# Optimization experiments

Hardware: AMD Instinct MI355X
Metric: run time of the kernel (lower is better)

The kernel has to match this reference:

```python
import jax, jax.numpy as jnp
import numpy as np

S, T, N, D, H, DT = 4, 4, 65536, 128, 128, 128


def setup_inputs() -> dict:
    key = jax.random.key(0)
    ks = jax.random.split(key, 9)
    inv_d = 1.0 / np.sqrt(D)
    inv_h = 1.0 / np.sqrt(H)
    return {
        "states": jax.random.normal(ks[0], (N, D), dtype=jnp.float32),
        "scores": jax.random.uniform(ks[1], (N, 1), dtype=jnp.float32),
        "type_ids": jax.random.randint(ks[2], (N,), 0, S, dtype=jnp.int32),
        "type_matching": jax.random.normal(ks[3], (S, T), dtype=jnp.float32),
        "W1": jax.random.normal(ks[4], (S, T, D, H), dtype=jnp.float32) * inv_d,
        "b1": jnp.zeros((S, T, H), dtype=jnp.float32),
        "W2": jax.random.normal(ks[5], (S, T, H, DT), dtype=jnp.float32) * inv_h,
        "b2": jnp.zeros((S, T, DT), dtype=jnp.float32),
        "C1": jax.random.normal(ks[6], (S, T, D, H), dtype=jnp.float32) * inv_d,
        "c1": jnp.zeros((S, T, H), dtype=jnp.float32),
        "C2": jax.random.normal(ks[7], (S, T, H, 1), dtype=jnp.float32) * inv_h,
        "c2": jnp.zeros((S, T, 1), dtype=jnp.float32),
    }


def reference(states, scores, type_ids, type_matching, W1, b1, W2, b2, C1, c1, C2, c2):
    """Batched MetaphorMorphism.forward with best_match_only=True.

    For each item with source type s: route to t* = argmax sigmoid(type_matching[s]),
    apply mapper MLP (D->H->DT, ReLU), classifier MLP (D->H->1, ReLU, sigmoid),
    new_score = min(score, classifier_out), item_prob = sigmoid(type_matching)[s, t*].
    """
    match_sig = jax.nn.sigmoid(type_matching)          # [S, T]
    best_t = jnp.argmax(type_matching, axis=1)         # [S] (argmax of sigmoid == argmax of logits)
    best_prob = match_sig[jnp.arange(S), best_t]       # [S]

    out_state = jnp.zeros((states.shape[0], W2.shape[-1]), dtype=states.dtype)
    out_score = jnp.zeros_like(scores)
    # loop over the small, fixed set of source types (structurally distinct experts)
    for s in range(S):
        t = best_t[s]
        h = jax.nn.relu(states @ W1[s, t] + b1[s, t])          # [N, H]
        y = h @ W2[s, t] + b2[s, t]                            # [N, DT]
        hc = jax.nn.relu(states @ C1[s, t] + c1[s, t])         # [N, H]
        cls = jax.nn.sigmoid(hc @ C2[s, t] + c2[s, t])         # [N, 1]
        new_score = jnp.minimum(scores, cls)                   # [N, 1]
        m = (type_ids == s)[:, None]
        out_state = jnp.where(m, y, out_state)
        out_score = jnp.where(m, new_score, out_score)
    item_prob = best_prob[type_ids]                            # [N]
    return out_state, out_score, item_prob
```

## Files before the change

### kernel.cpp

```cpp
#include <hip/hip_runtime.h>
#include <math.h>

#define Nn 65536

typedef short s16x8 __attribute__((ext_vector_type(8)));
typedef float f32x4 __attribute__((ext_vector_type(4)));
typedef unsigned int u32;

__device__ __forceinline__ unsigned short f2bf(float x) {
    u32 u = __float_as_uint(x);
    u += 0x7FFFu + ((u >> 16) & 1u);
    return (unsigned short)(u >> 16);
}

__device__ __forceinline__ int best_t_for(const float* __restrict__ tm, int s, float* mOut) {
    float m = tm[s * 4];
    int am = 0;
#pragma unroll
    for (int j = 1; j < 4; ++j) {
        float v = tm[s * 4 + j];
        if (v > m) { m = v; am = j; }
    }
    if (mOut) *mOut = m;
    return am;
}

__global__ void k_prep(const int* __restrict__ type_ids, const float* __restrict__ tm,
                       const float* __restrict__ W1, const float* __restrict__ W2,
                       const float* __restrict__ C1,
                       int* __restrict__ counts, int* __restrict__ buckets,
                       unsigned short* __restrict__ wbf, float* __restrict__ out_prob) {
    const int tid = threadIdx.x;
    if (blockIdx.x < 256) {
        __shared__ float prob[4];
        __shared__ int waveCnt[4][4];
        __shared__ int waveBase[4][4];
        if (tid < 4) {
            float m;
            best_t_for(tm, tid, &m);
            prob[tid] = 1.f / (1.f + expf(-m));
        }
        __syncthreads();
        const int gid = blockIdx.x * 256 + tid;
        const int id = type_ids[gid];
        out_prob[gid] = prob[id];
        const int lane = tid & 63;
        const int wvv = tid >> 6;
        const unsigned long long lt = (1ull << lane) - 1ull;
        int myPrefix = 0;
#pragma unroll
        for (int sv = 0; sv < 4; ++sv) {
            unsigned long long m = __ballot(id == sv);
            if (id == sv) myPrefix = (int)__popcll(m & lt);
            if (lane == 0) waveCnt[wvv][sv] = (int)__popcll(m);
        }
        __syncthreads();
        if (tid < 4) {
            const int sv = tid;
            int c0 = waveCnt[0][sv], c1 = waveCnt[1][sv];
            int c2_ = waveCnt[2][sv], c3 = waveCnt[3][sv];
            int tot = c0 + c1 + c2_ + c3;
            u32 old = atomicCAS((u32*)&counts[sv], 0xAAAAAAAAu, (u32)tot);
            int b = (old == 0xAAAAAAAAu) ? 0 : atomicAdd(&counts[sv], tot);
            waveBase[0][sv] = b;
            waveBase[1][sv] = b + c0;
            waveBase[2][sv] = b + c0 + c1;
            waveBase[3][sv] = b + c0 + c1 + c2_;
        }
        __syncthreads();
        buckets[id * Nn + waveBase[wvv][id] + myPrefix] = gid;
    } else {
        int u = (blockIdx.x - 256) * 256 + tid;
        int mat = u >> 11;
        int rr = u & 2047;
        int f = rr >> 6, lane = rr & 63;
        int kk = f >> 3, n8 = f & 7;
        int q = lane >> 4, l15 = lane & 15;
        int sm = mat / 3, w = mat - sm * 3;
        int t = best_t_for(tm, sm, nullptr);
        const float* src = (w == 0) ? W1 : (w == 1) ? W2 : C1;
        const float* sp = src + (((sm * 4 + t) << 14) + n8 * 16 + l15);
        int k0 = kk * 32 + q * 8;
        s16x8 o;
#pragma unroll
        for (int j = 0; j < 8; ++j) o[j] = (short)f2bf(sp[(k0 + j) * 128]);
        *(s16x8*)(wbf + (size_t)u * 8) = o;
    }
}

__global__ __launch_bounds__(512, 4) void k_main(
    const float* __restrict__ states, const float* __restrict__ scores,
    const float* __restrict__ b1g, const float* __restrict__ b2g, const float* __restrict__ c1g,
    const float* __restrict__ tm, const float* __restrict__ C2, const float* __restrict__ c2,
    const int* __restrict__ counts, const int* __restrict__ buckets,
    const unsigned short* __restrict__ wbf,
    float* __restrict__ out_state, float* __restrict__ out_score)
{
    __shared__ __align__(16) unsigned short Abuf[64 * 128];
    __shared__ __align__(16) unsigned short Hbuf[64 * 128];
    __shared__ int gIdxLds[64];
    __shared__ float scoreLds[64];
    __shared__ float pLds[8][64];

    const int s = blockIdx.y;
    const int cnt = counts[s];
    const int ntiles = (cnt + 63) >> 6;
    const int bx = blockIdx.x;
    if (bx >= ntiles) return;
    const int t = threadIdx.x;
    const int tt = best_t_for(tm, s, nullptr);
    const int stIdx = s * 4 + tt;

    const int lane = t & 63;
    const int wv = t >> 6;
    const int l15 = lane & 15;
    const int quad = lane >> 4;
    const int myRow = t >> 3;
    const int q8 = t & 7;
    const int col = wv * 16 + l15;

    const float b1v = b1g[stIdx * 128 + col];
    const float b2v = b2g[stIdx * 128 + col];
    const float c1v = c1g[stIdx * 128 + col];
    const float c2w = C2[stIdx * 128 + col];
    const float c2s = c2[stIdx];
    const int* bkt = buckets + s * Nn;
    const unsigned short* wb = wbf + (size_t)s * 3 * 16384;

    s16x8 wf[3][4];
#pragma unroll
    for (int m = 0; m < 3; ++m)
#pragma unroll
        for (int kk = 0; kk < 4; ++kk)
            wf[m][kk] = *(const s16x8*)(wb + m * 16384 +
                (size_t)((kk * 8 + wv) * 64 + lane) * 8);

    auto gemm = [&](const unsigned short* Ab, const s16x8 (&wfm)[4], f32x4 acc[4]) {
#pragma unroll
        for (int mg = 0; mg < 4; ++mg) acc[mg] = f32x4{0.f, 0.f, 0.f, 0.f};
#pragma unroll
        for (int kk = 0; kk < 4; ++kk) {
            const int colsw = (kk * 32 + quad * 8 + l15 * 8) & 127;
            s16x8 af[4];
#pragma unroll
            for (int mg = 0; mg < 4; ++mg)
                af[mg] = *(const s16x8*)(Ab + (mg * 16 + l15) * 128 + colsw);
#pragma unroll
            for (int mg = 0; mg < 4; ++mg)
                acc[mg] = __builtin_amdgcn_mfma_f32_16x16x32_bf16(
                    af[mg], wfm[kk], acc[mg], 0, 0, 0);
        }
    };

    f32x4 acc[4];
    for (int tile = bx; tile < ntiles; tile += gridDim.x) {
        if (tile != bx) __syncthreads();

        {
            int gr = tile * 64 + myRow;
            int g = (gr < cnt) ? bkt[gr] : -1;
            if (q8 == 0) {
                gIdxLds[myRow] = g;
                scoreLds[myRow] = (g >= 0) ? scores[g] : 0.f;
            }
            unsigned short* dstRow = &Abuf[myRow * 128];
            const int rot = (myRow & 15) << 3;
            if (g >= 0) {
                const float4* sp = (const float4*)(states + (size_t)g * 128 + q8 * 16);
                float4 v[4];
#pragma unroll
                for (int i = 0; i < 4; ++i) v[i] = sp[i];
#pragma unroll
                for (int i = 0; i < 4; ++i) {
                    int c = (q8 * 16 + i * 4 + rot) & 127;
                    ushort4 o;
                    o.x = f2bf(v[i].x); o.y = f2bf(v[i].y);
                    o.z = f2bf(v[i].z); o.w = f2bf(v[i].w);
                    *(ushort4*)(dstRow + c) = o;
                }
            } else {
#pragma unroll
                for (int i = 0; i < 4; ++i) {
                    int c = (q8 * 16 + i * 4 + rot) & 127;
                    *(ushort4*)(dstRow + c) = ushort4{0, 0, 0, 0};
                }
            }
        }
        __syncthreads();

        gemm(Abuf, wf[0], acc);
#pragma unroll
        for (int mg = 0; mg < 4; ++mg)
#pragma unroll
            for (int r = 0; r < 4; ++r) {
                int row = mg * 16 + quad * 4 + r;
                float v = fmaxf(acc[mg][r] + b1v, 0.f);
                Hbuf[row * 128 + ((col + ((row & 15) << 3)) & 127)] = f2bf(v);
            }
        __syncthreads();

        gemm(Hbuf, wf[1], acc);
#pragma unroll
        for (int mg = 0; mg < 4; ++mg) {
            int gr4[4];
#pragma unroll
            for (int r = 0; r < 4; ++r) gr4[r] = gIdxLds[mg * 16 + quad * 4 + r];
#pragma unroll
            for (int r = 0; r < 4; ++r)
                if (gr4[r] >= 0) out_state[(size_t)gr4[r] * 128 + col] = acc[mg][r] + b2v;
        }

        gemm(Abuf, wf[2], acc);
        {
            float part[4][4];
#pragma unroll
            for (int mg = 0; mg < 4; ++mg)
#pragma unroll
                for (int r = 0; r < 4; ++r)
                    part[mg][r] = fmaxf(acc[mg][r] + c1v, 0.f) * c2w;
#pragma unroll
            for (int off = 1; off < 16; off <<= 1)
#pragma unroll
                for (int mg = 0; mg < 4; ++mg)
#pragma unroll
                    for (int r = 0; r < 4; ++r)
                        part[mg][r] += __shfl_xor(part[mg][r], off, 64);
            if (l15 == 0) {
#pragma unroll
                for (int mg = 0; mg < 4; ++mg)
#pragma unroll
                    for (int r = 0; r < 4; ++r)
                        pLds[wv][mg * 16 + quad * 4 + r] = part[mg][r];
            }
        }
        __syncthreads();

        if (t < 64) {
            int eg = gIdxLds[t];
            if (eg >= 0) {
                float tot = pLds[0][t] + pLds[1][t] + pLds[2][t] + pLds[3][t]
                          + pLds[4][t] + pLds[5][t] + pLds[6][t] + pLds[7][t] + c2s;
                float cls = 1.f / (1.f + expf(-tot));
                out_score[eg] = fminf(scoreLds[t], cls);
            }
        }
    }
}

extern "C" void kernel_launch(void* const* d_in, const int* in_sizes, int n_in,
                              void* d_out, int out_size, void* d_ws, size_t ws_size,
                              hipStream_t stream) {
    const float* states = (const float*)d_in[0];
    const float* scores = (const float*)d_in[1];
    const int*   type_ids = (const int*)d_in[2];
    const float* tm = (const float*)d_in[3];
    const float* W1 = (const float*)d_in[4];
    const float* b1 = (const float*)d_in[5];
    const float* W2 = (const float*)d_in[6];
    const float* b2 = (const float*)d_in[7];
    const float* C1 = (const float*)d_in[8];
    const float* c1 = (const float*)d_in[9];
    const float* C2 = (const float*)d_in[10];
    const float* c2 = (const float*)d_in[11];

    char* ws = (char*)d_ws;
    int*   counts  = (int*)(ws + 0);
    int*   buckets = (int*)(ws + 4096);
    unsigned short* wbf = (unsigned short*)(ws + 1052672);

    float* out_state = (float*)d_out;
    float* out_score = out_state + (size_t)Nn * 128;
    float* out_prob  = out_score + Nn;

    k_prep<<<352, 256, 0, stream>>>(type_ids, tm, W1, W2, C1, counts, buckets, wbf, out_prob);
    k_main<<<dim3(128, 4), 512, 0, stream>>>(states, scores, b1, b2, c1,
        tm, C2, c2, counts, buckets, wbf, out_state, out_score);
}
```

Measured before the change: 133.4 us.

## Replace global bucketing with per-block local type segmentation in fused kernel

```diff
diff --git a/kernel.cpp b/kernel.cpp
--- a/kernel.cpp
+++ b/kernel.cpp
@@ -25,92 +25,46 @@
     return am;
 }
 
-__global__ void k_prep(const int* __restrict__ type_ids, const float* __restrict__ tm,
-                       const float* __restrict__ W1, const float* __restrict__ W2,
-                       const float* __restrict__ C1,
-                       int* __restrict__ counts, int* __restrict__ buckets,
-                       unsigned short* __restrict__ wbf, float* __restrict__ out_prob) {
-    const int tid = threadIdx.x;
-    if (blockIdx.x < 256) {
-        __shared__ float prob[4];
-        __shared__ int waveCnt[4][4];
-        __shared__ int waveBase[4][4];
-        if (tid < 4) {
-            float m;
-            best_t_for(tm, tid, &m);
-            prob[tid] = 1.f / (1.f + expf(-m));
-        }
-        __syncthreads();
-        const int gid = blockIdx.x * 256 + tid;
-        const int id = type_ids[gid];
-        out_prob[gid] = prob[id];
-        const int lane = tid & 63;
-        const int wvv = tid >> 6;
-        const unsigned long long lt = (1ull << lane) - 1ull;
-        int myPrefix = 0;
-#pragma unroll
-        for (int sv = 0; sv < 4; ++sv) {
-            unsigned long long m = __ballot(id == sv);
-            if (id == sv) myPrefix = (int)__popcll(m & lt);
-            if (lane == 0) waveCnt[wvv][sv] = (int)__popcll(m);
-        }
-        __syncthreads();
-        if (tid < 4) {
-            const int sv = tid;
-            int c0 = waveCnt[0][sv], c1 = waveCnt[1][sv];
-            int c2_ = waveCnt[2][sv], c3 = waveCnt[3][sv];
-            int tot = c0 + c1 + c2_ + c3;
-            u32 old = atomicCAS((u32*)&counts[sv], 0xAAAAAAAAu, (u32)tot);
-            int b = (old == 0xAAAAAAAAu) ? 0 : atomicAdd(&counts[sv], tot);
-            waveBase[0][sv] = b;
-            waveBase[1][sv] = b + c0;
-            waveBase[2][sv] = b + c0 + c1;
-            waveBase[3][sv] = b + c0 + c1 + c2_;
-        }
-        __syncthreads();
-        buckets[id * Nn + waveBase[wvv][id] + myPrefix] = gid;
-    } else {
-        int u = (blockIdx.x - 256) * 256 + tid;
-        int mat = u >> 11;
-        int rr = u & 2047;
-        int f = rr >> 6, lane = rr & 63;
-        int kk = f >> 3, n8 = f & 7;
-        int q = lane >> 4, l15 = lane & 15;
-        int sm = mat / 3, w = mat - sm * 3;
-        int t = best_t_for(tm, sm, nullptr);
-        const float* src = (w == 0) ? W1 : (w == 1) ? W2 : C1;
-        const float* sp = src + (((sm * 4 + t) << 14) + n8 * 16 + l15);
-        int k0 = kk * 32 + q * 8;
-        s16x8 o;
-#pragma unroll
-        for (int j = 0; j < 8; ++j) o[j] = (short)f2bf(sp[(k0 + j) * 128]);
-        *(s16x8*)(wbf + (size_t)u * 8) = o;
-    }
-}
-
-__global__ __launch_bounds__(512, 4) void k_main(
+__global__ void k_prepw(const float* __restrict__ tm,
+                        const float* __restrict__ W1, const float* __restrict__ W2,
+                        const float* __restrict__ C1, unsigned short* __restrict__ wbf) {
+    int u = blockIdx.x * 256 + threadIdx.x;
+    int mat = u >> 11;
+    int rr = u & 2047;
+    int f = rr >> 6, lane = rr & 63;
+    int kk = f >> 3, n8 = f & 7;
+    int q = lane >> 4, l15 = lane & 15;
+    int sm = mat / 3, w = mat - sm * 3;
+    int t = best_t_for(tm, sm, nullptr);
+    const float* src = (w == 0) ? W1 : (w == 1) ? W2 : C1;
+    const float* sp = src + (((sm * 4 + t) << 14) + n8 * 16 + l15);
+    int k0 = kk * 32 + q * 8;
+    s16x8 o;
+#pragma unroll
+    for (int j = 0; j < 8; ++j) o[j] = (short)f2bf(sp[(k0 + j) * 128]);
+    *(s16x8*)(wbf + (size_t)u * 8) = o;
+}
+
+__global__ __launch_bounds__(512, 4) void k_fused(
     const float* __restrict__ states, const float* __restrict__ scores,
-    const float* __restrict__ b1g, const float* __restrict__ b2g, const float* __restrict__ c1g,
-    const float* __restrict__ tm, const float* __restrict__ C2, const float* __restrict__ c2,
-    const int* __restrict__ counts, const int* __restrict__ buckets,
-    const unsigned short* __restrict__ wbf,
-    float* __restrict__ out_state, float* __restrict__ out_score)
+    const int* __restrict__ type_ids, const float* __restrict__ tm,
+    const float* __restrict__ b1g, const float* __restrict__ b2g,
+    const float* __restrict__ c1g, const float* __restrict__ C2,
+    const float* __restrict__ c2, const unsigned short* __restrict__ wbf,
+    float* __restrict__ out_state, float* __restrict__ out_score,
+    float* __restrict__ out_prob)
 {
     __shared__ __align__(16) unsigned short Abuf[64 * 128];
-    __shared__ __align__(16) unsigned short Hbuf[64 * 128];
-    __shared__ int gIdxLds[64];
+    __shared__ __align__(16) unsigned short Hbuf[112 * 128];
+    __shared__ int permLds[112];
+    __shared__ int segTypeLds[8];
+    __shared__ int Gs;
     __shared__ float scoreLds[64];
-    __shared__ float pLds[8][64];
-
-    const int s = blockIdx.y;
-    const int cnt = counts[s];
-    const int ntiles = (cnt + 63) >> 6;
-    const int bx = blockIdx.x;
-    if (bx >= ntiles) return;
+    __shared__ float pLds[8][112];
+    __shared__ float c2sL[4];
+
     const int t = threadIdx.x;
-    const int tt = best_t_for(tm, s, nullptr);
-    const int stIdx = s * 4 + tt;
-
+    const int gid0 = blockIdx.x * 64;
     const int lane = t & 63;
     const int wv = t >> 6;
     const int l15 = lane & 15;
@@ -119,130 +73,168 @@
     const int q8 = t & 7;
     const int col = wv * 16 + l15;
 
-    const float b1v = b1g[stIdx * 128 + col];
-    const float b2v = b2g[stIdx * 128 + col];
-    const float c1v = c1g[stIdx * 128 + col];
-    const float c2w = C2[stIdx * 128 + col];
-    const float c2s = c2[stIdx];
-    const int* bkt = buckets + s * Nn;
-    const unsigned short* wb = wbf + (size_t)s * 3 * 16384;
-
-    s16x8 wf[3][4];
-#pragma unroll
-    for (int m = 0; m < 3; ++m)
+    int stIdx4[4];
+#pragma unroll
+    for (int s = 0; s < 4; ++s) stIdx4[s] = s * 4 + best_t_for(tm, s, nullptr);
+    float b1vA[4], b2vA[4], c1vA[4], c2wA[4];
+#pragma unroll
+    for (int s = 0; s < 4; ++s) {
+        b1vA[s] = b1g[stIdx4[s] * 128 + col];
+        b2vA[s] = b2g[stIdx4[s] * 128 + col];
+        c1vA[s] = c1g[stIdx4[s] * 128 + col];
+        c2wA[s] = C2[stIdx4[s] * 128 + col];
+    }
+    if (t < 4) c2sL[t] = c2[stIdx4[t]];
+
+    {
+        const int g = gid0 + myRow;
+        const float4* sp = (const float4*)(states + (size_t)g * 128 + q8 * 16);
+        float4 v[4];
+#pragma unroll
+        for (int i = 0; i < 4; ++i) v[i] = sp[i];
+        unsigned short* dstRow = &Abuf[myRow * 128];
+        const int rot = (myRow & 15) << 3;
+#pragma unroll
+        for (int i = 0; i < 4; ++i) {
+            int c = (q8 * 16 + i * 4 + rot) & 127;
+            ushort4 o;
+            o.x = f2bf(v[i].x); o.y = f2bf(v[i].y);
+            o.z = f2bf(v[i].z); o.w = f2bf(v[i].w);
+            *(ushort4*)(dstRow + c) = o;
+        }
+    }
+
+    if (t < 64) {
+        int ty = type_ids[gid0 + t];
+        scoreLds[t] = scores[gid0 + t];
+        float m = tm[ty * 4];
+#pragma unroll
+        for (int j = 1; j < 4; ++j) m = fmaxf(m, tm[ty * 4 + j]);
+        out_prob[gid0 + t] = 1.f / (1.f + expf(-m));
+
+        unsigned long long m0 = __ballot(ty == 0);
+        unsigned long long m1 = __ballot(ty == 1);
+        unsigned long long m2 = __ballot(ty == 2);
+        unsigned long long m3 = __ballot(ty == 3);
+        int c0 = (int)__popcll(m0), c1 = (int)__popcll(m1);
+        int c2_ = (int)__popcll(m2), c3 = (int)__popcll(m3);
+        int ns0 = (c0 + 15) >> 4, ns1 = (c1 + 15) >> 4;
+        int ns2 = (c2_ + 15) >> 4, ns3 = (c3 + 15) >> 4;
+        int pb1 = ns0 * 16, pb2 = pb1 + ns1 * 16, pb3 = pb2 + ns2 * 16;
+        permLds[t] = -1;
+        if (t < 48) permLds[64 + t] = -1;
+        unsigned long long lt = (1ull << t) - 1ull;
+        int pb = (ty == 0) ? 0 : (ty == 1) ? pb1 : (ty == 2) ? pb2 : pb3;
+        unsigned long long mm = (ty == 0) ? m0 : (ty == 1) ? m1 : (ty == 2) ? m2 : m3;
+        permLds[pb + (int)__popcll(mm & lt)] = t;
+        if (t < 8) {
+            int st = (t < ns0) ? 0 : (t < ns0 + ns1) ? 1 : (t < ns0 + ns1 + ns2) ? 2 : 3;
+            segTypeLds[t] = st;
+        }
+        if (t == 0) Gs = ns0 + ns1 + ns2 + ns3;
+    }
+    __syncthreads();
+    const int G = Gs;
+
+    const unsigned short* __restrict__ wbase = wbf;
+    auto loadWf = [&](int m, int sty, s16x8 wf[4]) {
+        const unsigned short* wb = wbase + ((size_t)sty * 3 + m) * 16384;
 #pragma unroll
         for (int kk = 0; kk < 4; ++kk)
-            wf[m][kk] = *(const s16x8*)(wb + m * 16384 +
-                (size_t)((kk * 8 + wv) * 64 + lane) * 8);
-
-    auto gemm = [&](const unsigned short* Ab, const s16x8 (&wfm)[4], f32x4 acc[4]) {
-#pragma unroll
-        for (int mg = 0; mg < 4; ++mg) acc[mg] = f32x4{0.f, 0.f, 0.f, 0.f};
+            wf[kk] = *(const s16x8*)(wb + (size_t)((kk * 8 + wv) * 64 + lane) * 8);
+    };
+    auto gemmA = [&](int g, const s16x8 wf[4]) -> f32x4 {
+        f32x4 acc = {0.f, 0.f, 0.f, 0.f};
+        int pRow = permLds[g * 16 + l15];
+        int rbase = ((pRow >= 0) ? pRow : 0) * 128;
+        int rot = (pRow & 15) << 3;
 #pragma unroll
         for (int kk = 0; kk < 4; ++kk) {
-            const int colsw = (kk * 32 + quad * 8 + l15 * 8) & 127;
-            s16x8 af[4];
-#pragma unroll
-            for (int mg = 0; mg < 4; ++mg)
-                af[mg] = *(const s16x8*)(Ab + (mg * 16 + l15) * 128 + colsw);
-#pragma unroll
-            for (int mg = 0; mg < 4; ++mg)
-                acc[mg] = __builtin_amdgcn_mfma_f32_16x16x32_bf16(
-                    af[mg], wfm[kk], acc[mg], 0, 0, 0);
-        }
+            s16x8 af = *(const s16x8*)(Abuf + rbase + ((kk * 32 + quad * 8 + rot) & 127));
+            if (pRow < 0) af = s16x8{0, 0, 0, 0, 0, 0, 0, 0};
+            acc = __builtin_amdgcn_mfma_f32_16x16x32_bf16(af, wf[kk], acc, 0, 0, 0);
+        }
+        return acc;
     };
-
-    f32x4 acc[4];
-    for (int tile = bx; tile < ntiles; tile += gridDim.x) {
-        if (tile != bx) __syncthreads();
-
-        {
-            int gr = tile * 64 + myRow;
-            int g = (gr < cnt) ? bkt[gr] : -1;
-            if (q8 == 0) {
-                gIdxLds[myRow] = g;
-                scoreLds[myRow] = (g >= 0) ? scores[g] : 0.f;
-            }
-            unsigned short* dstRow = &Abuf[myRow * 128];
-            const int rot = (myRow & 15) << 3;
-            if (g >= 0) {
-                const float4* sp = (const float4*)(states + (size_t)g * 128 + q8 * 16);
-                float4 v[4];
-#pragma unroll
-                for (int i = 0; i < 4; ++i) v[i] = sp[i];
-#pragma unroll
-                for (int i = 0; i < 4; ++i) {
-                    int c = (q8 * 16 + i * 4 + rot) & 127;
-                    ushort4 o;
-                    o.x = f2bf(v[i].x); o.y = f2bf(v[i].y);
-                    o.z = f2bf(v[i].z); o.w = f2bf(v[i].w);
-                    *(ushort4*)(dstRow + c) = o;
-                }
-            } else {
-#pragma unroll
-                for (int i = 0; i < 4; ++i) {
-                    int c = (q8 * 16 + i * 4 + rot) & 127;
-                    *(ushort4*)(dstRow + c) = ushort4{0, 0, 0, 0};
-                }
-            }
-        }
-        __syncthreads();
-
-        gemm(Abuf, wf[0], acc);
-#pragma unroll
-        for (int mg = 0; mg < 4; ++mg)
+    auto gemmH = [&](int g, const s16x8 wf[4]) -> f32x4 {
+        f32x4 acc = {0.f, 0.f, 0.f, 0.f};
+        const unsigned short* hb = Hbuf + (g * 16 + l15) * 128;
+#pragma unroll
+        for (int kk = 0; kk < 4; ++kk) {
+            s16x8 af = *(const s16x8*)(hb + ((kk * 32 + quad * 8 + (l15 << 3)) & 127));
+            acc = __builtin_amdgcn_mfma_f32_16x16x32_bf16(af, wf[kk], acc, 0, 0, 0);
+        }
+        return acc;
+    };
+
+    s16x8 wfP[2][4];
+
+    loadWf(0, segTypeLds[0], wfP[0]);
+#pragma unroll
+    for (int g = 0; g < 7; ++g) {
+        if (g < G) {
+            if (g + 1 < G) loadWf(0, segTypeLds[g + 1], wfP[(g + 1) & 1]);
+            f32x4 a = gemmA(g, wfP[g & 1]);
+            int sty = segTypeLds[g];
+            float bb = (sty == 0) ? b1vA[0] : (sty == 1) ? b1vA[1] : (sty == 2) ? b1vA[2] : b1vA[3];
 #pragma unroll
             for (int r = 0; r < 4; ++r) {
-                int row = mg * 16 + quad * 4 + r;
-                float v = fmaxf(acc[mg][r] + b1v, 0.f);
+                int row = g * 16 + quad * 4 + r;
+                float v = fmaxf(a[r] + bb, 0.f);
                 Hbuf[row * 128 + ((col + ((row & 15) << 3)) & 127)] = f2bf(v);
             }
-        __syncthreads();
-
-        gemm(Hbuf, wf[1], acc);
-#pragma unroll
-        for (int mg = 0; mg < 4; ++mg) {
-            int gr4[4];
-#pragma unroll
-            for (int r = 0; r < 4; ++r) gr4[r] = gIdxLds[mg * 16 + quad * 4 + r];
-#pragma unroll
-            for (int r = 0; r < 4; ++r)
-                if (gr4[r] >= 0) out_state[(size_t)gr4[r] * 128 + col] = acc[mg][r] + b2v;
-        }
-
-        gemm(Abuf, wf[2], acc);
-        {
-            float part[4][4];
-#pragma unroll
-            for (int mg = 0; mg < 4; ++mg)
-#pragma unroll
-                for (int r = 0; r < 4; ++r)
-                    part[mg][r] = fmaxf(acc[mg][r] + c1v, 0.f) * c2w;
+        }
+    }
+    __syncthreads();
+
+    loadWf(1, segTypeLds[0], wfP[0]);
+#pragma unroll
+    for (int g = 0; g < 7; ++g) {
+        if (g < G) {
+            if (g + 1 < G) loadWf(1, segTypeLds[g + 1], wfP[(g + 1) & 1]);
+            f32x4 a = gemmH(g, wfP[g & 1]);
+            int sty = segTypeLds[g];
+            float bb = (sty == 0) ? b2vA[0] : (sty == 1) ? b2vA[1] : (sty == 2) ? b2vA[2] : b2vA[3];
+#pragma unroll
+            for (int r = 0; r < 4; ++r) {
+                int p = permLds[g * 16 + quad * 4 + r];
+                if (p >= 0) out_state[(size_t)(gid0 + p) * 128 + col] = a[r] + bb;
+            }
+        }
+    }
+
+    loadWf(2, segTypeLds[0], wfP[0]);
+#pragma unroll
+    for (int g = 0; g < 7; ++g) {
+        if (g < G) {
+            if (g + 1 < G) loadWf(2, segTypeLds[g + 1], wfP[(g + 1) & 1]);
+            f32x4 a = gemmA(g, wfP[g & 1]);
+            int sty = segTypeLds[g];
+            float cv = (sty == 0) ? c1vA[0] : (sty == 1) ? c1vA[1] : (sty == 2) ? c1vA[2] : c1vA[3];
+            float cw = (sty == 0) ? c2wA[0] : (sty == 1) ? c2wA[1] : (sty == 2) ? c2wA[2] : c2wA[3];
+            float part[4];
+#pragma unroll
+            for (int r = 0; r < 4; ++r) part[r] = fmaxf(a[r] + cv, 0.f) * cw;
 #pragma unroll
             for (int off = 1; off < 16; off <<= 1)
 #pragma unroll
-                for (int mg = 0; mg < 4; ++mg)
-#pragma unroll
-                    for (int r = 0; r < 4; ++r)
-                        part[mg][r] += __shfl_xor(part[mg][r], off, 64);
+                for (int r = 0; r < 4; ++r) part[r] += __shfl_xor(part[r], off, 64);
             if (l15 == 0) {
 #pragma unroll
-                for (int mg = 0; mg < 4; ++mg)
-#pragma unroll
-                    for (int r = 0; r < 4; ++r)
-                        pLds[wv][mg * 16 + quad * 4 + r] = part[mg][r];
+                for (int r = 0; r < 4; ++r) pLds[wv][g * 16 + quad * 4 + r] = part[r];
             }
         }
-        __syncthreads();
-
-        if (t < 64) {
-            int eg = gIdxLds[t];
-            if (eg >= 0) {
-                float tot = pLds[0][t] + pLds[1][t] + pLds[2][t] + pLds[3][t]
-                          + pLds[4][t] + pLds[5][t] + pLds[6][t] + pLds[7][t] + c2s;
-                float cls = 1.f / (1.f + expf(-tot));
-                out_score[eg] = fminf(scoreLds[t], cls);
-            }
+    }
+    __syncthreads();
+
+    if (t < 112 && t < G * 16) {
+        int p = permLds[t];
+        if (p >= 0) {
+            float tot = pLds[0][t] + pLds[1][t] + pLds[2][t] + pLds[3][t]
+                      + pLds[4][t] + pLds[5][t] + pLds[6][t] + pLds[7][t]
+                      + c2sL[segTypeLds[t >> 4]];
+            float cls = 1.f / (1.f + expf(-tot));
+            out_score[gid0 + p] = fminf(scoreLds[p], cls);
         }
     }
 }
@@ -263,16 +255,13 @@
     const float* C2 = (const float*)d_in[10];
     const float* c2 = (const float*)d_in[11];
 
-    char* ws = (char*)d_ws;
-    int*   counts  = (int*)(ws + 0);
-    int*   buckets = (int*)(ws + 4096);
-    unsigned short* wbf = (unsigned short*)(ws + 1052672);
+    unsigned short* wbf = (unsigned short*)d_ws;
 
     float* out_state = (float*)d_out;
     float* out_score = out_state + (size_t)Nn * 128;
     float* out_prob  = out_score + Nn;
 
-    k_prep<<<352, 256, 0, stream>>>(type_ids, tm, W1, W2, C1, counts, buckets, wbf, out_prob);
-    k_main<<<dim3(128, 4), 512, 0, stream>>>(states, scores, b1, b2, c1,
-        tm, C2, c2, counts, buckets, wbf, out_state, out_score);
-}
+    k_prepw<<<96, 256, 0, stream>>>(tm, W1, W2, C1, wbf);
+    k_fused<<<1024, 512, 0, stream>>>(states, scores, type_ids, tm, b1, b2, c1,
+        C2, c2, wbf, out_state, out_score, out_prob);
+}
```

Result: no change. 136.1 us (+2.0%).
